# Kernel tuning notes

Measured on AMD Instinct MI355X. Metric: run time of the kernel, lower is better.

## Reference

```python
import jax, jax.numpy as jnp
import numpy as np

N_NODES = 50000
N_EDGES = 800000
IN_F = 256
OUT_F = 64


def setup_inputs() -> dict:
    key = jax.random.key(0)
    k1, k2, k3, k4, k5 = jax.random.split(key, 5)
    x = jax.random.normal(k1, (N_NODES, IN_F), dtype=jnp.float32)
    # xavier-uniform-like init for weight
    limit = float(np.sqrt(6.0 / (IN_F + OUT_F)))
    weight = jax.random.uniform(k2, (IN_F, OUT_F), dtype=jnp.float32, minval=-limit, maxval=limit)
    bias = jnp.zeros((1, OUT_F), dtype=jnp.float32)
    edge_weight = jax.random.uniform(k3, (N_EDGES,), dtype=jnp.float32)
    edge_src = jax.random.randint(k4, (N_EDGES,), 0, N_NODES, dtype=jnp.int32)
    edge_dst = jax.random.randint(k5, (N_EDGES,), 0, N_NODES, dtype=jnp.int32)
    return {"x": x, "weight": weight, "bias": bias,
            "edge_weight": edge_weight, "edge_src": edge_src, "edge_dst": edge_dst}


def reference(x, weight, bias, edge_weight, edge_src, edge_dst):
    # in_features (256) > out_features (64): transform first, then propagate.
    h = x @ weight                                  # [N, out]
    # spmm with COO adjacency: out[dst] += w_e * h[src]
    msgs = h[edge_src] * edge_weight[:, None]       # [E, out]
    out = jax.ops.segment_sum(msgs, edge_dst, num_segments=x.shape[0])  # [N, out]
    return out + bias
```

## Files before the change

kernel.cpp:

```cpp
#include <hip/hip_runtime.h>
#include <hip/hip_bf16.h>

#define N_NODES 50000
#define N_EDGES 800000
#define IN_F 256
#define OUT_F 64

#define CAP 64
#define NBKT 128
#define DST_PER_BKT 391
#define BKT_CAP 6912

typedef __attribute__((ext_vector_type(8))) short short8;
typedef __attribute__((ext_vector_type(4))) float f32x4;

static __device__ __forceinline__ ushort f2bf(float v) {
    __hip_bfloat16 b = __float2bfloat16(v);
    return *(ushort*)&b;
}

__global__ __launch_bounds__(256) void gc_prep(const float* __restrict__ W,
                                               ushort* __restrict__ Wb,
                                               int* __restrict__ cursor) {
    const int g = blockIdx.x * 256 + threadIdx.x;
    if (g < NBKT) cursor[g] = 0;
    {
        const int s = g >> 9;
        const int kk = (g >> 6) & 7;
        const int lane = g & 63;
        const int n = s * 16 + (lane & 15);
        const int kb = kk * 32 + (lane >> 4) * 8;
#pragma unroll
        for (int j = 0; j < 8; ++j)
            Wb[(size_t)g * 8 + j] = f2bf(W[(kb + j) * OUT_F + n]);
    }
}

__global__ __launch_bounds__(256) void gc_bucket(const int* __restrict__ esrc,
                                                 const int* __restrict__ edst,
                                                 const float* __restrict__ ew,
                                                 int* __restrict__ cursor,
                                                 uint2* __restrict__ arena) {
    __shared__ int hist[NBKT];
    __shared__ int base[NBKT];
    const int t = threadIdx.x;
    if (t < NBKT) hist[t] = 0;
    __syncthreads();

    const int e0 = blockIdx.x * 2048 + t * 8;
    const bool valid = e0 < N_EDGES;
    int b[8], loff[8];
    uint2 ent[8];
    if (valid) {
        const int4 sa = *(const int4*)(esrc + e0);
        const int4 sb = *(const int4*)(esrc + e0 + 4);
        const int4 da = *(const int4*)(edst + e0);
        const int4 db = *(const int4*)(edst + e0 + 4);
        const float4 wa = *(const float4*)(ew + e0);
        const float4 wb = *(const float4*)(ew + e0 + 4);
        const int ds[8] = {da.x, da.y, da.z, da.w, db.x, db.y, db.z, db.w};
        const int ss[8] = {sa.x, sa.y, sa.z, sa.w, sb.x, sb.y, sb.z, sb.w};
        const float wf[8] = {wa.x, wa.y, wa.z, wa.w, wb.x, wb.y, wb.z, wb.w};
#pragma unroll
        for (int j = 0; j < 8; ++j) {
            b[j] = ds[j] / DST_PER_BKT;
            ent[j].x = (unsigned)ds[j];
            ent[j].y = ((unsigned)f2bf(wf[j]) << 16) | (unsigned)(ss[j] & 0xFFFF);
            loff[j] = atomicAdd(&hist[b[j]], 1);
        }
    }
    __syncthreads();
    if (t < NBKT) {
        const int hc = hist[t];
        base[t] = hc ? atomicAdd(&cursor[t], hc) : 0;
    }
    __syncthreads();
    if (valid) {
#pragma unroll
        for (int j = 0; j < 8; ++j)
            arena[(size_t)b[j] * BKT_CAP + base[b[j]] + loff[j]] = ent[j];
    }
}

__global__ __launch_bounds__(512) void gc_place2(const uint2* __restrict__ arena,
                                                 const int* __restrict__ cursor,
                                                 int* __restrict__ cnt,
                                                 unsigned int* __restrict__ slots) {
    __shared__ int lcnt[DST_PER_BKT];
    const int b = blockIdx.x;
    const int t = threadIdx.x;
    const int dbase = b * DST_PER_BKT;

    for (int i = t; i < DST_PER_BKT; i += 512) lcnt[i] = 0;
    __syncthreads();

    const int n = min(cursor[b], BKT_CAP);
    const uint2* __restrict__ p = arena + (size_t)b * BKT_CAP;
    for (int i = t; i < n; i += 512) {
        const uint2 ent = p[i];
        const int pos = atomicAdd(&lcnt[ent.x - dbase], 1);
        if (pos < CAP) slots[(size_t)ent.x * CAP + pos] = ent.y;
    }
    __syncthreads();

    for (int i = t; i < DST_PER_BKT; i += 512) {
        const int d = dbase + i;
        if (d < N_NODES) cnt[d] = lcnt[i];
    }
}

__global__ __launch_bounds__(256) void gc_gemm(const float* __restrict__ x,
                                               const ushort* __restrict__ Wb,
                                               ushort* __restrict__ h) {
    __shared__ ushort xs[32 * 264];
    const int t = threadIdx.x;
    const int nbase = blockIdx.x * 32;

    {
#pragma unroll
        for (int i = 0; i < 8; ++i) {
            const int idx = t + i * 256;
            const int node = idx >> 6;
            const int c4 = idx & 63;
            int gnode = nbase + node;
            if (gnode >= N_NODES) gnode = N_NODES - 1;
            const float4 v = ((const float4*)x)[(size_t)gnode * 64 + c4];
            ushort4 bv;
            bv.x = f2bf(v.x); bv.y = f2bf(v.y); bv.z = f2bf(v.z); bv.w = f2bf(v.w);
            *(ushort4*)&xs[node * 264 + c4 * 4] = bv;
        }
    }

    const int s = t >> 6;
    const int lane = t & 63;
    const int m = lane & 15;
    const int quad = lane >> 4;

    short8 bfrag[8];
#pragma unroll
    for (int kk = 0; kk < 8; ++kk)
        bfrag[kk] = *(const short8*)(Wb + ((size_t)(s * 8 + kk) * 64 + lane) * 8);

    __syncthreads();

    f32x4 acc0 = {0.f, 0.f, 0.f, 0.f};
    f32x4 acc1 = {0.f, 0.f, 0.f, 0.f};
#pragma unroll
    for (int kk = 0; kk < 8; ++kk) {
        const short8 a0 = *(const short8*)&xs[m * 264 + kk * 32 + quad * 8];
        const short8 a1 = *(const short8*)&xs[(16 + m) * 264 + kk * 32 + quad * 8];
        acc0 = __builtin_amdgcn_mfma_f32_16x16x32_bf16(a0, bfrag[kk], acc0, 0, 0, 0);
        acc1 = __builtin_amdgcn_mfma_f32_16x16x32_bf16(a1, bfrag[kk], acc1, 0, 0, 0);
    }

#pragma unroll
    for (int r = 0; r < 4; ++r) {
        const int row0 = nbase + quad * 4 + r;
        const int row1 = row0 + 16;
        if (row0 < N_NODES) h[(size_t)row0 * OUT_F + s * 16 + m] = f2bf(acc0[r]);
        if (row1 < N_NODES) h[(size_t)row1 * OUT_F + s * 16 + m] = f2bf(acc1[r]);
    }
}

__global__ __launch_bounds__(256) void gc_gather(const ushort* __restrict__ h,
                                                 const unsigned int* __restrict__ slots,
                                                 const int* __restrict__ cnt,
                                                 const float* __restrict__ bias,
                                                 float* __restrict__ out) {
    const int wid = __builtin_amdgcn_readfirstlane(
        (int)((blockIdx.x * 256 + threadIdx.x) >> 6));
    const int f = threadIdx.x & 63;
    const int d0 = wid * 8;
    if (d0 >= N_NODES) return;

    const int4 ca = *(const int4*)(cnt + d0);
    const int4 cb = *(const int4*)(cnt + d0 + 4);
    const int dg0 = min(ca.x, CAP), dg1 = min(ca.y, CAP);
    const int dg2 = min(ca.z, CAP), dg3 = min(ca.w, CAP);
    const int dg4 = min(cb.x, CAP), dg5 = min(cb.y, CAP);
    const int dg6 = min(cb.z, CAP), dg7 = min(cb.w, CAP);
    const int mdeg = max(max(max(dg0, dg1), max(dg2, dg3)),
                         max(max(dg4, dg5), max(dg6, dg7)));

    const unsigned sw0 = (f < dg0) ? slots[(size_t)(d0 + 0) * CAP + f] : 0u;
    const unsigned sw1 = (f < dg1) ? slots[(size_t)(d0 + 1) * CAP + f] : 0u;
    const unsigned sw2 = (f < dg2) ? slots[(size_t)(d0 + 2) * CAP + f] : 0u;
    const unsigned sw3 = (f < dg3) ? slots[(size_t)(d0 + 3) * CAP + f] : 0u;
    const unsigned sw4 = (f < dg4) ? slots[(size_t)(d0 + 4) * CAP + f] : 0u;
    const unsigned sw5 = (f < dg5) ? slots[(size_t)(d0 + 5) * CAP + f] : 0u;
    const unsigned sw6 = (f < dg6) ? slots[(size_t)(d0 + 6) * CAP + f] : 0u;
    const unsigned sw7 = (f < dg7) ? slots[(size_t)(d0 + 7) * CAP + f] : 0u;

    const float b = bias[f];
    float a0 = b, a1 = b, a2 = b, a3 = b, a4 = b, a5 = b, a6 = b, a7 = b;

    const ushort* __restrict__ hf = h + f;

#define ROWLD(sw, l) \
    hf[(size_t)((unsigned)__builtin_amdgcn_readlane((int)(sw), (l)) & 0xFFFFu) * OUT_F]
#define WBITS(sw, l) \
    __uint_as_float((unsigned)__builtin_amdgcn_readlane((int)(sw), (l)) & 0xFFFF0000u)

    for (int i0 = 0; i0 < mdeg; i0 += 8) {
        unsigned hv0[8], hv1[8], hv2[8], hv3[8], hv4[8], hv5[8], hv6[8], hv7[8];
#pragma unroll
        for (int j = 0; j < 8; ++j) {
            const int l = i0 + j;
            hv0[j] = ROWLD(sw0, l);
            hv1[j] = ROWLD(sw1, l);
            hv2[j] = ROWLD(sw2, l);
            hv3[j] = ROWLD(sw3, l);
            hv4[j] = ROWLD(sw4, l);
            hv5[j] = ROWLD(sw5, l);
            hv6[j] = ROWLD(sw6, l);
            hv7[j] = ROWLD(sw7, l);
        }
#pragma unroll
        for (int j = 0; j < 8; ++j) {
            const int l = i0 + j;
            a0 += WBITS(sw0, l) * __uint_as_float(hv0[j] << 16);
            a1 += WBITS(sw1, l) * __uint_as_float(hv1[j] << 16);
            a2 += WBITS(sw2, l) * __uint_as_float(hv2[j] << 16);
            a3 += WBITS(sw3, l) * __uint_as_float(hv3[j] << 16);
            a4 += WBITS(sw4, l) * __uint_as_float(hv4[j] << 16);
            a5 += WBITS(sw5, l) * __uint_as_float(hv5[j] << 16);
            a6 += WBITS(sw6, l) * __uint_as_float(hv6[j] << 16);
            a7 += WBITS(sw7, l) * __uint_as_float(hv7[j] << 16);
        }
    }
#undef ROWLD
#undef WBITS

    out[(size_t)(d0 + 0) * OUT_F + f] = a0;
    out[(size_t)(d0 + 1) * OUT_F + f] = a1;
    out[(size_t)(d0 + 2) * OUT_F + f] = a2;
    out[(size_t)(d0 + 3) * OUT_F + f] = a3;
    out[(size_t)(d0 + 4) * OUT_F + f] = a4;
    out[(size_t)(d0 + 5) * OUT_F + f] = a5;
    out[(size_t)(d0 + 6) * OUT_F + f] = a6;
    out[(size_t)(d0 + 7) * OUT_F + f] = a7;
}

extern "C" void kernel_launch(void* const* d_in, const int* in_sizes, int n_in,
                              void* d_out, int out_size, void* d_ws, size_t ws_size,
                              hipStream_t stream) {
    const float* x    = (const float*)d_in[0];
    const float* W    = (const float*)d_in[1];
    const float* bias = (const float*)d_in[2];
    const float* ew   = (const float*)d_in[3];
    const int* src    = (const int*)d_in[4];
    const int* dst    = (const int*)d_in[5];
    float* out = (float*)d_out;

    char* ws = (char*)d_ws;
    ushort* h           = (ushort*)ws;
    int* cnt            = (int*)(ws + 6400000);
    unsigned int* slots = (unsigned int*)(ws + 6600000);
    ushort* Wb          = (ushort*)(ws + 19400000);
    int* cursor         = (int*)(ws + 19432768);
    uint2* arena        = (uint2*)(ws + 19433280);

    gc_prep<<<8, 256, 0, stream>>>(W, Wb, cursor);
    gc_bucket<<<391, 256, 0, stream>>>(src, dst, ew, cursor, arena);
    gc_place2<<<NBKT, 512, 0, stream>>>(arena, cursor, cnt, slots);
    gc_gemm<<<1563, 256, 0, stream>>>(x, Wb, h);
    gc_gather<<<1563, 256, 0, stream>>>(h, slots, cnt, bias, out);
}
```

Measured before the change: 144.1 us.

## Merge bucket and GEMM into one launch; vectorize gather with 16-byte row loads

The edge bucketing and the bf16 GEMM now run as separate block ranges of one kernel, so the independent stages can overlap and one launch is saved. The gather is rewritten so each wave handles 4 destinations. Each lane loads a 16-byte chunk of a source row, so 8 edges are processed in parallel per wave, and partial sums are then reduced with cross-lane shuffles. Row fetches become wider and fewer, at the cost of shuffle reductions and more registers for accumulators.

```diff
diff --git a/kernel.cpp b/kernel.cpp
--- a/kernel.cpp
+++ b/kernel.cpp
@@ -36,86 +36,60 @@
     }
 }
 
-__global__ __launch_bounds__(256) void gc_bucket(const int* __restrict__ esrc,
-                                                 const int* __restrict__ edst,
-                                                 const float* __restrict__ ew,
-                                                 int* __restrict__ cursor,
-                                                 uint2* __restrict__ arena) {
+__global__ __launch_bounds__(256) void gc_mid(const float* __restrict__ x,
+                                              const ushort* __restrict__ Wb,
+                                              ushort* __restrict__ h,
+                                              const int* __restrict__ esrc,
+                                              const int* __restrict__ edst,
+                                              const float* __restrict__ ew,
+                                              int* __restrict__ cursor,
+                                              uint2* __restrict__ arena) {
+    __shared__ ushort xs[32 * 264];
     __shared__ int hist[NBKT];
     __shared__ int base[NBKT];
     const int t = threadIdx.x;
-    if (t < NBKT) hist[t] = 0;
-    __syncthreads();
-
-    const int e0 = blockIdx.x * 2048 + t * 8;
-    const bool valid = e0 < N_EDGES;
-    int b[8], loff[8];
-    uint2 ent[8];
-    if (valid) {
-        const int4 sa = *(const int4*)(esrc + e0);
-        const int4 sb = *(const int4*)(esrc + e0 + 4);
-        const int4 da = *(const int4*)(edst + e0);
-        const int4 db = *(const int4*)(edst + e0 + 4);
-        const float4 wa = *(const float4*)(ew + e0);
-        const float4 wb = *(const float4*)(ew + e0 + 4);
-        const int ds[8] = {da.x, da.y, da.z, da.w, db.x, db.y, db.z, db.w};
-        const int ss[8] = {sa.x, sa.y, sa.z, sa.w, sb.x, sb.y, sb.z, sb.w};
-        const float wf[8] = {wa.x, wa.y, wa.z, wa.w, wb.x, wb.y, wb.z, wb.w};
-#pragma unroll
-        for (int j = 0; j < 8; ++j) {
-            b[j] = ds[j] / DST_PER_BKT;
-            ent[j].x = (unsigned)ds[j];
-            ent[j].y = ((unsigned)f2bf(wf[j]) << 16) | (unsigned)(ss[j] & 0xFFFF);
-            loff[j] = atomicAdd(&hist[b[j]], 1);
-        }
-    }
-    __syncthreads();
-    if (t < NBKT) {
-        const int hc = hist[t];
-        base[t] = hc ? atomicAdd(&cursor[t], hc) : 0;
-    }
-    __syncthreads();
-    if (valid) {
-#pragma unroll
-        for (int j = 0; j < 8; ++j)
-            arena[(size_t)b[j] * BKT_CAP + base[b[j]] + loff[j]] = ent[j];
-    }
-}
-
-__global__ __launch_bounds__(512) void gc_place2(const uint2* __restrict__ arena,
-                                                 const int* __restrict__ cursor,
-                                                 int* __restrict__ cnt,
-                                                 unsigned int* __restrict__ slots) {
-    __shared__ int lcnt[DST_PER_BKT];
-    const int b = blockIdx.x;
-    const int t = threadIdx.x;
-    const int dbase = b * DST_PER_BKT;
-
-    for (int i = t; i < DST_PER_BKT; i += 512) lcnt[i] = 0;
-    __syncthreads();
-
-    const int n = min(cursor[b], BKT_CAP);
-    const uint2* __restrict__ p = arena + (size_t)b * BKT_CAP;
-    for (int i = t; i < n; i += 512) {
-        const uint2 ent = p[i];
-        const int pos = atomicAdd(&lcnt[ent.x - dbase], 1);
-        if (pos < CAP) slots[(size_t)ent.x * CAP + pos] = ent.y;
-    }
-    __syncthreads();
-
-    for (int i = t; i < DST_PER_BKT; i += 512) {
-        const int d = dbase + i;
-        if (d < N_NODES) cnt[d] = lcnt[i];
-    }
-}
-
-__global__ __launch_bounds__(256) void gc_gemm(const float* __restrict__ x,
-                                               const ushort* __restrict__ Wb,
-                                               ushort* __restrict__ h) {
-    __shared__ ushort xs[32 * 264];
-    const int t = threadIdx.x;
-    const int nbase = blockIdx.x * 32;
-
+
+    if (blockIdx.x < 391) {
+        if (t < NBKT) hist[t] = 0;
+        __syncthreads();
+
+        const int e0 = blockIdx.x * 2048 + t * 8;
+        const bool valid = e0 < N_EDGES;
+        int b[8], loff[8];
+        uint2 ent[8];
+        if (valid) {
+            const int4 sa = *(const int4*)(esrc + e0);
+            const int4 sb = *(const int4*)(esrc + e0 + 4);
+            const int4 da = *(const int4*)(edst + e0);
+            const int4 db = *(const int4*)(edst + e0 + 4);
+            const float4 wa = *(const float4*)(ew + e0);
+            const float4 wb = *(const float4*)(ew + e0 + 4);
+            const int ds[8] = {da.x, da.y, da.z, da.w, db.x, db.y, db.z, db.w};
+            const int ss[8] = {sa.x, sa.y, sa.z, sa.w, sb.x, sb.y, sb.z, sb.w};
+            const float wf[8] = {wa.x, wa.y, wa.z, wa.w, wb.x, wb.y, wb.z, wb.w};
+#pragma unroll
+            for (int j = 0; j < 8; ++j) {
+                b[j] = ds[j] / DST_PER_BKT;
+                ent[j].x = (unsigned)ds[j];
+                ent[j].y = ((unsigned)f2bf(wf[j]) << 16) | (unsigned)(ss[j] & 0xFFFF);
+                loff[j] = atomicAdd(&hist[b[j]], 1);
+            }
+        }
+        __syncthreads();
+        if (t < NBKT) {
+            const int hc = hist[t];
+            base[t] = hc ? atomicAdd(&cursor[t], hc) : 0;
+        }
+        __syncthreads();
+        if (valid) {
+#pragma unroll
+            for (int j = 0; j < 8; ++j)
+                arena[(size_t)b[j] * BKT_CAP + base[b[j]] + loff[j]] = ent[j];
+        }
+        return;
+    }
+
+    const int nbase = (blockIdx.x - 391) * 32;
     {
 #pragma unroll
         for (int i = 0; i < 8; ++i) {
@@ -162,83 +136,117 @@
     }
 }
 
+__global__ __launch_bounds__(512) void gc_place2(const uint2* __restrict__ arena,
+                                                 const int* __restrict__ cursor,
+                                                 int* __restrict__ cnt,
+                                                 unsigned int* __restrict__ slots) {
+    __shared__ int lcnt[DST_PER_BKT];
+    const int b = blockIdx.x;
+    const int t = threadIdx.x;
+    const int dbase = b * DST_PER_BKT;
+
+    for (int i = t; i < DST_PER_BKT; i += 512) lcnt[i] = 0;
+    __syncthreads();
+
+    const int n = min(cursor[b], BKT_CAP);
+    const uint2* __restrict__ p = arena + (size_t)b * BKT_CAP;
+    for (int i = t; i < n; i += 512) {
+        const uint2 ent = p[i];
+        const int pos = atomicAdd(&lcnt[ent.x - dbase], 1);
+        if (pos < CAP) slots[(size_t)ent.x * CAP + pos] = ent.y;
+    }
+    __syncthreads();
+
+    for (int i = t; i < DST_PER_BKT; i += 512) {
+        const int d = dbase + i;
+        if (d < N_NODES) cnt[d] = lcnt[i];
+    }
+}
+
 __global__ __launch_bounds__(256) void gc_gather(const ushort* __restrict__ h,
                                                  const unsigned int* __restrict__ slots,
                                                  const int* __restrict__ cnt,
                                                  const float* __restrict__ bias,
                                                  float* __restrict__ out) {
-    const int wid = __builtin_amdgcn_readfirstlane(
-        (int)((blockIdx.x * 256 + threadIdx.x) >> 6));
-    const int f = threadIdx.x & 63;
-    const int d0 = wid * 8;
-    if (d0 >= N_NODES) return;
-
-    const int4 ca = *(const int4*)(cnt + d0);
-    const int4 cb = *(const int4*)(cnt + d0 + 4);
-    const int dg0 = min(ca.x, CAP), dg1 = min(ca.y, CAP);
-    const int dg2 = min(ca.z, CAP), dg3 = min(ca.w, CAP);
-    const int dg4 = min(cb.x, CAP), dg5 = min(cb.y, CAP);
-    const int dg6 = min(cb.z, CAP), dg7 = min(cb.w, CAP);
-    const int mdeg = max(max(max(dg0, dg1), max(dg2, dg3)),
-                         max(max(dg4, dg5), max(dg6, dg7)));
-
-    const unsigned sw0 = (f < dg0) ? slots[(size_t)(d0 + 0) * CAP + f] : 0u;
-    const unsigned sw1 = (f < dg1) ? slots[(size_t)(d0 + 1) * CAP + f] : 0u;
-    const unsigned sw2 = (f < dg2) ? slots[(size_t)(d0 + 2) * CAP + f] : 0u;
-    const unsigned sw3 = (f < dg3) ? slots[(size_t)(d0 + 3) * CAP + f] : 0u;
-    const unsigned sw4 = (f < dg4) ? slots[(size_t)(d0 + 4) * CAP + f] : 0u;
-    const unsigned sw5 = (f < dg5) ? slots[(size_t)(d0 + 5) * CAP + f] : 0u;
-    const unsigned sw6 = (f < dg6) ? slots[(size_t)(d0 + 6) * CAP + f] : 0u;
-    const unsigned sw7 = (f < dg7) ? slots[(size_t)(d0 + 7) * CAP + f] : 0u;
-
-    const float b = bias[f];
-    float a0 = b, a1 = b, a2 = b, a3 = b, a4 = b, a5 = b, a6 = b, a7 = b;
-
-    const ushort* __restrict__ hf = h + f;
-
-#define ROWLD(sw, l) \
-    hf[(size_t)((unsigned)__builtin_amdgcn_readlane((int)(sw), (l)) & 0xFFFFu) * OUT_F]
-#define WBITS(sw, l) \
-    __uint_as_float((unsigned)__builtin_amdgcn_readlane((int)(sw), (l)) & 0xFFFF0000u)
+    const int wid = (blockIdx.x * 256 + threadIdx.x) >> 6;
+    const int l = threadIdx.x & 63;
+    const int d0 = wid * 4;
+
+    const int4 c4 = *(const int4*)(cnt + d0);
+    const int dg0 = min(c4.x, CAP), dg1 = min(c4.y, CAP);
+    const int dg2 = min(c4.z, CAP), dg3 = min(c4.w, CAP);
+    const int mdeg = max(max(dg0, dg1), max(dg2, dg3));
+
+    const unsigned sw0 = (l < dg0) ? slots[(size_t)(d0 + 0) * CAP + l] : 0u;
+    const unsigned sw1 = (l < dg1) ? slots[(size_t)(d0 + 1) * CAP + l] : 0u;
+    const unsigned sw2 = (l < dg2) ? slots[(size_t)(d0 + 2) * CAP + l] : 0u;
+    const unsigned sw3 = (l < dg3) ? slots[(size_t)(d0 + 3) * CAP + l] : 0u;
+
+    const int es = l >> 3;
+    const int fb = l & 7;
+
+    float a0[8] = {0,0,0,0,0,0,0,0}, a1[8] = {0,0,0,0,0,0,0,0};
+    float a2[8] = {0,0,0,0,0,0,0,0}, a3[8] = {0,0,0,0,0,0,0,0};
+
+    const uint4* __restrict__ hb = (const uint4*)h;
 
     for (int i0 = 0; i0 < mdeg; i0 += 8) {
-        unsigned hv0[8], hv1[8], hv2[8], hv3[8], hv4[8], hv5[8], hv6[8], hv7[8];
-#pragma unroll
-        for (int j = 0; j < 8; ++j) {
-            const int l = i0 + j;
-            hv0[j] = ROWLD(sw0, l);
-            hv1[j] = ROWLD(sw1, l);
-            hv2[j] = ROWLD(sw2, l);
-            hv3[j] = ROWLD(sw3, l);
-            hv4[j] = ROWLD(sw4, l);
-            hv5[j] = ROWLD(sw5, l);
-            hv6[j] = ROWLD(sw6, l);
-            hv7[j] = ROWLD(sw7, l);
-        }
-#pragma unroll
-        for (int j = 0; j < 8; ++j) {
-            const int l = i0 + j;
-            a0 += WBITS(sw0, l) * __uint_as_float(hv0[j] << 16);
-            a1 += WBITS(sw1, l) * __uint_as_float(hv1[j] << 16);
-            a2 += WBITS(sw2, l) * __uint_as_float(hv2[j] << 16);
-            a3 += WBITS(sw3, l) * __uint_as_float(hv3[j] << 16);
-            a4 += WBITS(sw4, l) * __uint_as_float(hv4[j] << 16);
-            a5 += WBITS(sw5, l) * __uint_as_float(hv5[j] << 16);
-            a6 += WBITS(sw6, l) * __uint_as_float(hv6[j] << 16);
-            a7 += WBITS(sw7, l) * __uint_as_float(hv7[j] << 16);
-        }
-    }
-#undef ROWLD
-#undef WBITS
-
-    out[(size_t)(d0 + 0) * OUT_F + f] = a0;
-    out[(size_t)(d0 + 1) * OUT_F + f] = a1;
-    out[(size_t)(d0 + 2) * OUT_F + f] = a2;
-    out[(size_t)(d0 + 3) * OUT_F + f] = a3;
-    out[(size_t)(d0 + 4) * OUT_F + f] = a4;
-    out[(size_t)(d0 + 5) * OUT_F + f] = a5;
-    out[(size_t)(d0 + 6) * OUT_F + f] = a6;
-    out[(size_t)(d0 + 7) * OUT_F + f] = a7;
+        const int ei = i0 + es;
+        const unsigned q0 = (unsigned)__shfl((int)sw0, ei);
+        const unsigned q1 = (unsigned)__shfl((int)sw1, ei);
+        const unsigned q2 = (unsigned)__shfl((int)sw2, ei);
+        const unsigned q3 = (unsigned)__shfl((int)sw3, ei);
+        const uint4 v0 = hb[(size_t)(q0 & 0xFFFFu) * 8 + fb];
+        const uint4 v1 = hb[(size_t)(q1 & 0xFFFFu) * 8 + fb];
+        const uint4 v2 = hb[(size_t)(q2 & 0xFFFFu) * 8 + fb];
+        const uint4 v3 = hb[(size_t)(q3 & 0xFFFFu) * 8 + fb];
+
+#define FMA8(acc, q, v)                                                       \
+    {                                                                         \
+        const float w_ = __uint_as_float((q) & 0xFFFF0000u);                  \
+        acc[0] = fmaf(w_, __uint_as_float((v).x << 16), acc[0]);              \
+        acc[1] = fmaf(w_, __uint_as_float((v).x & 0xFFFF0000u), acc[1]);      \
+        acc[2] = fmaf(w_, __uint_as_float((v).y << 16), acc[2]);              \
+        acc[3] = fmaf(w_, __uint_as_float((v).y & 0xFFFF0000u), acc[3]);      \
+        acc[4] = fmaf(w_, __uint_as_float((v).z << 16), acc[4]);              \
+        acc[5] = fmaf(w_, __uint_as_float((v).z & 0xFFFF0000u), acc[5]);      \
+        acc[6] = fmaf(w_, __uint_as_float((v).w << 16), acc[6]);              \
+        acc[7] = fmaf(w_, __uint_as_float((v).w & 0xFFFF0000u), acc[7]);      \
+    }
+        FMA8(a0, q0, v0);
+        FMA8(a1, q1, v1);
+        FMA8(a2, q2, v2);
+        FMA8(a3, q3, v3);
+#undef FMA8
+    }
+
+#pragma unroll
+    for (int k = 0; k < 8; ++k) {
+        a0[k] += __shfl_xor(a0[k], 8); a0[k] += __shfl_xor(a0[k], 16); a0[k] += __shfl_xor(a0[k], 32);
+        a1[k] += __shfl_xor(a1[k], 8); a1[k] += __shfl_xor(a1[k], 16); a1[k] += __shfl_xor(a1[k], 32);
+        a2[k] += __shfl_xor(a2[k], 8); a2[k] += __shfl_xor(a2[k], 16); a2[k] += __shfl_xor(a2[k], 32);
+        a3[k] += __shfl_xor(a3[k], 8); a3[k] += __shfl_xor(a3[k], 16); a3[k] += __shfl_xor(a3[k], 32);
+    }
+
+    if (l < 8) {
+        const float4 ba = ((const float4*)bias)[l * 2];
+        const float4 bb = ((const float4*)bias)[l * 2 + 1];
+#define STORE4(acc, d)                                                        \
+    {                                                                         \
+        float4 oa, ob;                                                        \
+        oa.x = acc[0] + ba.x; oa.y = acc[1] + ba.y;                           \
+        oa.z = acc[2] + ba.z; oa.w = acc[3] + ba.w;                           \
+        ob.x = acc[4] + bb.x; ob.y = acc[5] + bb.y;                           \
+        ob.z = acc[6] + bb.z; ob.w = acc[7] + bb.w;                           \
+        float4* op = (float4*)(out + (size_t)(d) * OUT_F + l * 8);            \
+        op[0] = oa; op[1] = ob;                                               \
+    }
+        STORE4(a0, d0 + 0);
+        STORE4(a1, d0 + 1);
+        STORE4(a2, d0 + 2);
+        STORE4(a3, d0 + 3);
+#undef STORE4
+    }
 }
 
 extern "C" void kernel_launch(void* const* d_in, const int* in_sizes, int n_in,
@@ -261,8 +269,7 @@
     uint2* arena        = (uint2*)(ws + 19433280);
 
     gc_prep<<<8, 256, 0, stream>>>(W, Wb, cursor);
-    gc_bucket<<<391, 256, 0, stream>>>(src, dst, ew, cursor, arena);
+    gc_mid<<<1954, 256, 0, stream>>>(x, Wb, h, src, dst, ew, cursor, arena);
     gc_place2<<<NBKT, 512, 0, stream>>>(arena, cursor, cnt, slots);
-    gc_gemm<<<1563, 256, 0, stream>>>(x, Wb, h);
-    gc_gather<<<1563, 256, 0, stream>>>(h, slots, cnt, bias, out);
-}
+    gc_gather<<<3125, 256, 0, stream>>>(h, slots, cnt, bias, out);
+}
```

After: 145.3 us. No clear change (+0.8%).

## Split h into feature halves and gather two edges per wave iteration

Applied to the files above, without the earlier changes.

The GEMM now writes h as two column-major halves of 32 features each, so each half is a compact [N,32] bf16 array. The gather launches twice as many blocks, one set per half, and within a wave lanes 0-31 and 32-63 handle alternating edges on the same 32 features, combining them with a cross-half shuffle at the end. This aims to halve the per-edge row footprint touched by each block, improve cache locality, and double the edge parallelism per wave, at the cost of reading slots and cnt twice. It also adds a bounds guard on arena writes in the bucketing kernel.

```diff
diff --git a/kernel.cpp b/kernel.cpp
--- a/kernel.cpp
+++ b/kernel.cpp
@@ -77,8 +77,11 @@
     __syncthreads();
     if (valid) {
 #pragma unroll
-        for (int j = 0; j < 8; ++j)
-            arena[(size_t)b[j] * BKT_CAP + base[b[j]] + loff[j]] = ent[j];
+        for (int j = 0; j < 8; ++j) {
+            const int pos = base[b[j]] + loff[j];
+            if (pos < BKT_CAP)
+                arena[(size_t)b[j] * BKT_CAP + pos] = ent[j];
+        }
     }
 }
 
@@ -153,12 +156,15 @@
         acc1 = __builtin_amdgcn_mfma_f32_16x16x32_bf16(a1, bfrag[kk], acc1, 0, 0, 0);
     }
 
+    const int hhalf = s >> 1;
+    const int hcol = (s & 1) * 16 + m;
+    ushort* __restrict__ hp = h + (size_t)hhalf * N_NODES * 32 + hcol;
 #pragma unroll
     for (int r = 0; r < 4; ++r) {
         const int row0 = nbase + quad * 4 + r;
         const int row1 = row0 + 16;
-        if (row0 < N_NODES) h[(size_t)row0 * OUT_F + s * 16 + m] = f2bf(acc0[r]);
-        if (row1 < N_NODES) h[(size_t)row1 * OUT_F + s * 16 + m] = f2bf(acc1[r]);
+        if (row0 < N_NODES) hp[(size_t)row0 * 32] = f2bf(acc0[r]);
+        if (row1 < N_NODES) hp[(size_t)row1 * 32] = f2bf(acc1[r]);
     }
 }
 
@@ -167,10 +173,12 @@
                                                  const int* __restrict__ cnt,
                                                  const float* __restrict__ bias,
                                                  float* __restrict__ out) {
-    const int wid = __builtin_amdgcn_readfirstlane(
-        (int)((blockIdx.x * 256 + threadIdx.x) >> 6));
-    const int f = threadIdx.x & 63;
-    const int d0 = wid * 8;
+    const int blk = blockIdx.x;
+    const int half = (blk >= 1563) ? 1 : 0;
+    const int grp = blk - half * 1563;
+    const int w = threadIdx.x >> 6;
+    const int l = threadIdx.x & 63;
+    const int d0 = (grp * 4 + w) * 8;
     if (d0 >= N_NODES) return;
 
     const int4 ca = *(const int4*)(cnt + d0);
@@ -182,63 +190,67 @@
     const int mdeg = max(max(max(dg0, dg1), max(dg2, dg3)),
                          max(max(dg4, dg5), max(dg6, dg7)));
 
-    const unsigned sw0 = (f < dg0) ? slots[(size_t)(d0 + 0) * CAP + f] : 0u;
-    const unsigned sw1 = (f < dg1) ? slots[(size_t)(d0 + 1) * CAP + f] : 0u;
-    const unsigned sw2 = (f < dg2) ? slots[(size_t)(d0 + 2) * CAP + f] : 0u;
-    const unsigned sw3 = (f < dg3) ? slots[(size_t)(d0 + 3) * CAP + f] : 0u;
-    const unsigned sw4 = (f < dg4) ? slots[(size_t)(d0 + 4) * CAP + f] : 0u;
-    const unsigned sw5 = (f < dg5) ? slots[(size_t)(d0 + 5) * CAP + f] : 0u;
-    const unsigned sw6 = (f < dg6) ? slots[(size_t)(d0 + 6) * CAP + f] : 0u;
-    const unsigned sw7 = (f < dg7) ? slots[(size_t)(d0 + 7) * CAP + f] : 0u;
-
-    const float b = bias[f];
-    float a0 = b, a1 = b, a2 = b, a3 = b, a4 = b, a5 = b, a6 = b, a7 = b;
-
-    const ushort* __restrict__ hf = h + f;
-
-#define ROWLD(sw, l) \
-    hf[(size_t)((unsigned)__builtin_amdgcn_readlane((int)(sw), (l)) & 0xFFFFu) * OUT_F]
-#define WBITS(sw, l) \
-    __uint_as_float((unsigned)__builtin_amdgcn_readlane((int)(sw), (l)) & 0xFFFF0000u)
+    const unsigned sw0 = (l < dg0) ? slots[(size_t)(d0 + 0) * CAP + l] : 0u;
+    const unsigned sw1 = (l < dg1) ? slots[(size_t)(d0 + 1) * CAP + l] : 0u;
+    const unsigned sw2 = (l < dg2) ? slots[(size_t)(d0 + 2) * CAP + l] : 0u;
+    const unsigned sw3 = (l < dg3) ? slots[(size_t)(d0 + 3) * CAP + l] : 0u;
+    const unsigned sw4 = (l < dg4) ? slots[(size_t)(d0 + 4) * CAP + l] : 0u;
+    const unsigned sw5 = (l < dg5) ? slots[(size_t)(d0 + 5) * CAP + l] : 0u;
+    const unsigned sw6 = (l < dg6) ? slots[(size_t)(d0 + 6) * CAP + l] : 0u;
+    const unsigned sw7 = (l < dg7) ? slots[(size_t)(d0 + 7) * CAP + l] : 0u;
+
+    const int hi = l >> 5;
+    const int c = l & 31;
+    const ushort* __restrict__ hb = h + (size_t)half * N_NODES * 32 + c;
+
+    float a0 = 0.f, a1 = 0.f, a2 = 0.f, a3 = 0.f;
+    float a4 = 0.f, a5 = 0.f, a6 = 0.f, a7 = 0.f;
 
     for (int i0 = 0; i0 < mdeg; i0 += 8) {
-        unsigned hv0[8], hv1[8], hv2[8], hv3[8], hv4[8], hv5[8], hv6[8], hv7[8];
-#pragma unroll
-        for (int j = 0; j < 8; ++j) {
-            const int l = i0 + j;
-            hv0[j] = ROWLD(sw0, l);
-            hv1[j] = ROWLD(sw1, l);
-            hv2[j] = ROWLD(sw2, l);
-            hv3[j] = ROWLD(sw3, l);
-            hv4[j] = ROWLD(sw4, l);
-            hv5[j] = ROWLD(sw5, l);
-            hv6[j] = ROWLD(sw6, l);
-            hv7[j] = ROWLD(sw7, l);
-        }
-#pragma unroll
-        for (int j = 0; j < 8; ++j) {
-            const int l = i0 + j;
-            a0 += WBITS(sw0, l) * __uint_as_float(hv0[j] << 16);
-            a1 += WBITS(sw1, l) * __uint_as_float(hv1[j] << 16);
-            a2 += WBITS(sw2, l) * __uint_as_float(hv2[j] << 16);
-            a3 += WBITS(sw3, l) * __uint_as_float(hv3[j] << 16);
-            a4 += WBITS(sw4, l) * __uint_as_float(hv4[j] << 16);
-            a5 += WBITS(sw5, l) * __uint_as_float(hv5[j] << 16);
-            a6 += WBITS(sw6, l) * __uint_as_float(hv6[j] << 16);
-            a7 += WBITS(sw7, l) * __uint_as_float(hv7[j] << 16);
-        }
-    }
-#undef ROWLD
-#undef WBITS
-
-    out[(size_t)(d0 + 0) * OUT_F + f] = a0;
-    out[(size_t)(d0 + 1) * OUT_F + f] = a1;
-    out[(size_t)(d0 + 2) * OUT_F + f] = a2;
-    out[(size_t)(d0 + 3) * OUT_F + f] = a3;
-    out[(size_t)(d0 + 4) * OUT_F + f] = a4;
-    out[(size_t)(d0 + 5) * OUT_F + f] = a5;
-    out[(size_t)(d0 + 6) * OUT_F + f] = a6;
-    out[(size_t)(d0 + 7) * OUT_F + f] = a7;
+#define PROC(sw, acc)                                                          \
+    {                                                                          \
+        unsigned q[4];                                                         \
+        ushort hv[4];                                                          \
+        _Pragma("unroll") for (int p = 0; p < 4; ++p)                          \
+        {                                                                      \
+            const int e = i0 + p * 2;                                          \
+            const int qlo = __builtin_amdgcn_readlane((int)(sw), e);           \
+            const int qhi = __builtin_amdgcn_readlane((int)(sw), e + 1);       \
+            q[p] = (unsigned)(hi ? qhi : qlo);                                 \
+            hv[p] = hb[(size_t)(q[p] & 0xFFFFu) * 32];                         \
+        }                                                                      \
+        _Pragma("unroll") for (int p = 0; p < 4; ++p)                          \
+            acc = fmaf(__uint_as_float(q[p] & 0xFFFF0000u),                    \
+                       __uint_as_float((unsigned)hv[p] << 16), acc);           \
+    }
+        PROC(sw0, a0)
+        PROC(sw1, a1)
+        PROC(sw2, a2)
+        PROC(sw3, a3)
+        PROC(sw4, a4)
+        PROC(sw5, a5)
+        PROC(sw6, a6)
+        PROC(sw7, a7)
+#undef PROC
+    }
+
+    a0 += __shfl_xor(a0, 32); a1 += __shfl_xor(a1, 32);
+    a2 += __shfl_xor(a2, 32); a3 += __shfl_xor(a3, 32);
+    a4 += __shfl_xor(a4, 32); a5 += __shfl_xor(a5, 32);
+    a6 += __shfl_xor(a6, 32); a7 += __shfl_xor(a7, 32);
+
+    if (l < 32) {
+        const float bf = bias[half * 32 + l];
+        float* __restrict__ ob = out + half * 32 + l;
+        ob[(size_t)(d0 + 0) * OUT_F] = a0 + bf;
+        ob[(size_t)(d0 + 1) * OUT_F] = a1 + bf;
+        ob[(size_t)(d0 + 2) * OUT_F] = a2 + bf;
+        ob[(size_t)(d0 + 3) * OUT_F] = a3 + bf;
+        ob[(size_t)(d0 + 4) * OUT_F] = a4 + bf;
+        ob[(size_t)(d0 + 5) * OUT_F] = a5 + bf;
+        ob[(size_t)(d0 + 6) * OUT_F] = a6 + bf;
+        ob[(size_t)(d0 + 7) * OUT_F] = a7 + bf;
+    }
 }
 
 extern "C" void kernel_launch(void* const* d_in, const int* in_sizes, int n_in,
@@ -264,5 +276,5 @@
     gc_bucket<<<391, 256, 0, stream>>>(src, dst, ew, cursor, arena);
     gc_place2<<<NBKT, 512, 0, stream>>>(arena, cursor, cnt, slots);
     gc_gemm<<<1563, 256, 0, stream>>>(x, Wb, h);
-    gc_gather<<<1563, 256, 0, stream>>>(h, slots, cnt, bias, out);
-}
+    gc_gather<<<3126, 256, 0, stream>>>(h, slots, cnt, bias, out);
+}
```

New measurement: 158.5 us. 1.1x slower.
